# Optimization experiments

Hardware: AMD Instinct MI355X
Metric: run time of the kernel (lower is better)

The kernel has to match this reference:

```python
import jax, jax.numpy as jnp
import numpy as np
import math

D_MODEL = 1024
N_HEADS = 16
HEAD_DIM = D_MODEL // N_HEADS
B = 2
S = 2048

def setup_inputs() -> dict:
    key = jax.random.key(0)
    ks = jax.random.split(key, 5)
    x = jax.random.normal(ks[0], (B, S, D_MODEL), dtype=jnp.float32)
    # causal lower-triangular mask, broadcastable to [B, H, S, S]
    mask = jnp.tril(jnp.ones((S, S), dtype=bool))[None, None, :, :]
    # qkv_proj: Linear(d_model, 3*d_model); out_proj: Linear(d_model, d_model)
    lim_qkv = 1.0 / math.sqrt(D_MODEL)
    Wqkv = jax.random.uniform(ks[1], (D_MODEL, 3 * D_MODEL), minval=-lim_qkv, maxval=lim_qkv, dtype=jnp.float32)
    bqkv = jax.random.uniform(ks[2], (3 * D_MODEL,), minval=-lim_qkv, maxval=lim_qkv, dtype=jnp.float32)
    Wo = jax.random.uniform(ks[3], (D_MODEL, D_MODEL), minval=-lim_qkv, maxval=lim_qkv, dtype=jnp.float32)
    bo = jax.random.uniform(ks[4], (D_MODEL,), minval=-lim_qkv, maxval=lim_qkv, dtype=jnp.float32)
    return {"x": x, "mask": mask, "Wqkv": Wqkv, "bqkv": bqkv, "Wo": Wo, "bo": bo}

def reference(x, mask, Wqkv, bqkv, Wo, bo):
    b, s, d = x.shape
    scale = math.sqrt(HEAD_DIM)
    qkv = x @ Wqkv + bqkv                                   # [b, s, 3d]
    qkv = qkv.reshape(b, s, 3, N_HEADS, HEAD_DIM)
    qkv = jnp.transpose(qkv, (2, 0, 3, 1, 4))               # [3, b, h, s, hd]
    q, k, v = qkv[0], qkv[1], qkv[2]
    scores = jnp.einsum("bhqd,bhkd->bhqk", q, k) / scale    # [b, h, s, s]
    scores = jnp.where(mask, scores, -jnp.inf)
    attn = jax.nn.softmax(scores, axis=-1)                  # dropout inactive (eval)
    out = jnp.einsum("bhqk,bhkd->bhqd", attn, v)            # [b, h, s, hd]
    out = jnp.transpose(out, (0, 2, 1, 3)).reshape(b, s, d)
    return out @ Wo + bo
```

## Files before the change

### kernel.cpp

```cpp
#include <hip/hip_runtime.h>
#include <stdint.h>

typedef __bf16 bf16x8 __attribute__((ext_vector_type(8)));
typedef float  f32x4  __attribute__((ext_vector_type(4)));

__device__ __forceinline__ float bf2f(ushort u) {
    union { uint i; float f; } v; v.i = ((uint)u) << 16; return v.f;
}
__device__ __forceinline__ ushort f2bf(float f) {
    union { uint i; float f; } v; v.f = f;
    uint i = v.i;
    uint r = (i + 0x7fffu + ((i >> 16) & 1u)) >> 16;
    return (ushort)r;
}
__device__ __forceinline__ ushort f2bf_t(float f) {
    union { uint i; float f; } v; v.f = f;
    return (ushort)(v.i >> 16);
}

__device__ __forceinline__ void gld16(const ushort* g, ushort* l) {
    __builtin_amdgcn_global_load_lds((const __attribute__((address_space(1))) uint*)g,
                                     (__attribute__((address_space(3))) uint*)l, 16, 0, 0);
}

#define D_MODEL 1024
#define N_HEADS 16
#define HEAD_DIM 64
#define BATCH 2
#define SEQ 2048
#define M_ROWS (BATCH * SEQ)
#define N_ITEMS 1024
#define SCALE_LOG2E 0.18033688f

__global__ __launch_bounds__(256) void cast_f32_bf16(
    const float* __restrict__ in, ushort* __restrict__ out, int n4)
{
    int i = blockIdx.x * 256 + threadIdx.x;
    if (i < n4) {
        float4 v = ((const float4*)in)[i];
        ushort4 o;
        o.x = f2bf(v.x); o.y = f2bf(v.y); o.z = f2bf(v.z); o.w = f2bf(v.w);
        ((ushort4*)out)[i] = o;
    }
}

__global__ __launch_bounds__(256) void transpose_f32_bf16(
    const float* __restrict__ in, ushort* __restrict__ out, int K, int N)
{
    __shared__ float tile[64][65];
    const int k0 = blockIdx.y << 6, n0 = blockIdx.x << 6;
    const int tid = threadIdx.x;
    {
        const int r  = tid >> 4;
        const int c4 = (tid & 15) * 4;
#pragma unroll
        for (int rr = 0; rr < 4; ++rr) {
            int kk = r + rr * 16;
            float4 v = *(const float4*)(in + (size_t)(k0 + kk) * N + n0 + c4);
            tile[kk][c4 + 0] = v.x; tile[kk][c4 + 1] = v.y;
            tile[kk][c4 + 2] = v.z; tile[kk][c4 + 3] = v.w;
        }
    }
    __syncthreads();
    {
        const int nn = tid & 63;
        const int ch = tid >> 6;
#pragma unroll
        for (int cc = 0; cc < 2; ++cc) {
            int k8 = (ch + cc * 4) * 8;
            ushort tmp[8] __attribute__((aligned(16)));
#pragma unroll
            for (int j = 0; j < 8; ++j) tmp[j] = f2bf(tile[k8 + j][nn]);
            *(uint4*)(out + (size_t)(n0 + nn) * K + k0 + k8) = *(const uint4*)tmp;
        }
    }
}

__global__ __launch_bounds__(256) void gemm_bt128(
    const ushort* __restrict__ A, const ushort* __restrict__ Bt,
    const float* __restrict__ bias, float* __restrict__ out,
    ushort* __restrict__ Qb, ushort* __restrict__ Kb, ushort* __restrict__ Vb,
    int M, int N, int K, int mode)
{
    __shared__ ushort As[128 * 32];
    __shared__ ushort Bs[128 * 32];
    const int tid = threadIdx.x, lane = tid & 63, w = tid >> 6;
    const int wr = w >> 1, wc = w & 1;
    const int m0 = blockIdx.y * 128, n0 = blockIdx.x * 128;
    const int quad = lane >> 4, r15 = lane & 15, q8 = quad * 8;

    f32x4 acc[4][4] = {};

    const int cb0 = w * 64;
    const int cb1 = 256 + w * 64;
    const int c0 = cb0 + lane, c1 = cb1 + lane;
    const int row0 = c0 >> 2, sc0 = (c0 & 3) * 8;
    const int row1 = c1 >> 2, sc1 = (c1 & 3) * 8;

    for (int k0 = 0; k0 < K; k0 += 32) {
        gld16(A  + (size_t)(m0 + row0) * K + k0 + sc0, As + cb0 * 8);
        gld16(A  + (size_t)(m0 + row1) * K + k0 + sc1, As + cb1 * 8);
        gld16(Bt + (size_t)(n0 + row0) * K + k0 + sc0, Bs + cb0 * 8);
        gld16(Bt + (size_t)(n0 + row1) * K + k0 + sc1, Bs + cb1 * 8);
        __syncthreads();
        bf16x8 af[4], bfv[4];
#pragma unroll
        for (int mt = 0; mt < 4; ++mt)
            af[mt] = *(const bf16x8*)&As[(wr * 64 + mt * 16 + r15) * 32 + q8];
#pragma unroll
        for (int nt = 0; nt < 4; ++nt)
            bfv[nt] = *(const bf16x8*)&Bs[(wc * 64 + nt * 16 + r15) * 32 + q8];
#pragma unroll
        for (int mt = 0; mt < 4; ++mt)
#pragma unroll
            for (int nt = 0; nt < 4; ++nt)
                acc[mt][nt] = __builtin_amdgcn_mfma_f32_16x16x32_bf16(af[mt], bfv[nt], acc[mt][nt], 0, 0, 0);
        __syncthreads();
    }

    const int q4 = quad * 4;
    float bv[4];
#pragma unroll
    for (int nt = 0; nt < 4; ++nt) bv[nt] = bias[n0 + wc * 64 + nt * 16 + r15];
#pragma unroll
    for (int mt = 0; mt < 4; ++mt) {
#pragma unroll
        for (int nt = 0; nt < 4; ++nt) {
#pragma unroll
            for (int r = 0; r < 4; ++r) {
                int m = m0 + wr * 64 + mt * 16 + q4 + r;
                int n = n0 + wc * 64 + nt * 16 + r15;
                float v = acc[mt][nt][r] + bv[nt];
                if (mode == 0) {
                    int which = n >> 10, nh = n & 1023;
                    int h = nh >> 6, d = nh & 63;
                    int b = m >> 11, s = m & 2047;
                    size_t dst = (((size_t)(b * N_HEADS + h)) * SEQ + s) * HEAD_DIM + d;
                    ushort* p = (which == 0) ? Qb : ((which == 1) ? Kb : Vb);
                    p[dst] = f2bf(v);
                } else {
                    out[(size_t)m * N + n] = v;
                }
            }
        }
    }
}

__global__ __launch_bounds__(256) void attn_mfma(
    const ushort* __restrict__ Q, const ushort* __restrict__ K,
    const ushort* __restrict__ V, ushort* __restrict__ Out,
    int* __restrict__ counter)
{
    __shared__ ushort Ks[2][64 * 72];
    __shared__ ushort Vt[2][64 * 72];
    __shared__ ushort Ps[4][16 * 72];
    __shared__ int s_item;

    const int tid  = threadIdx.x;
    const int lane = tid & 63;
    const int w    = tid >> 6;
    const int quad = lane >> 4;
    const int r15  = lane & 15;
    const int q8   = quad * 8;

    const int srow = tid >> 2;
    const int scol = (tid & 3) * 16;
    const int kp = tid & 31;
    const int dg = tid >> 5;

    for (;;) {
        __syncthreads();
        if (tid == 0) s_item = atomicAdd(counter, 1);
        __syncthreads();
        const int item = s_item;
        if (item >= N_ITEMS) break;

        const int qblk = 31 - (item >> 5);
        const int bh   = item & 31;
        const int q0   = qblk * 64;
        const size_t base = (size_t)bh * SEQ * HEAD_DIM;
        const int wq0  = q0 + w * 16;
        const int ntiles = qblk + 1;

        bf16x8 qf[2];
        {
            const ushort* qrow = Q + base + (size_t)(wq0 + r15) * HEAD_DIM;
            qf[0] = *(const bf16x8*)(qrow + q8);
            qf[1] = *(const bf16x8*)(qrow + 32 + q8);
        }

        f32x4 o_acc[4] = {};
        float l_lane[4] = {0.f, 0.f, 0.f, 0.f};

        uint4 kr0, kr1, vr0, vr1;
        {
            const ushort* kpt = K + base + (size_t)srow * HEAD_DIM + scol;
            kr0 = *(const uint4*)kpt; kr1 = *(const uint4*)(kpt + 8);
            const ushort* vpt = V + base + (size_t)(2 * kp) * HEAD_DIM + dg * 8;
            vr0 = *(const uint4*)vpt; vr1 = *(const uint4*)(vpt + HEAD_DIM);
        }
        {
            ushort* ks = &Ks[0][0];
            *(uint4*)&ks[srow * 72 + scol]     = kr0;
            *(uint4*)&ks[srow * 72 + scol + 8] = kr1;
            const ushort* a = (const ushort*)&vr0;
            const ushort* b = (const ushort*)&vr1;
            uint* vt32 = (uint*)&Vt[0][0];
#pragma unroll
            for (int j = 0; j < 8; ++j)
                vt32[(dg * 8 + j) * 36 + ((kp + 4 * dg) & 31)] = (uint)a[j] | ((uint)b[j] << 16);
        }
        if (ntiles > 1) {
            const ushort* kpt = K + base + (size_t)(64 + srow) * HEAD_DIM + scol;
            kr0 = *(const uint4*)kpt; kr1 = *(const uint4*)(kpt + 8);
            const ushort* vpt = V + base + (size_t)(64 + 2 * kp) * HEAD_DIM + dg * 8;
            vr0 = *(const uint4*)vpt; vr1 = *(const uint4*)(vpt + HEAD_DIM);
        }

        for (int t = 0; t < ntiles; ++t) {
            __syncthreads();
            if (t + 1 < ntiles) {
                const int b1 = (t + 1) & 1;
                ushort* ks = &Ks[b1][0];
                *(uint4*)&ks[srow * 72 + scol]     = kr0;
                *(uint4*)&ks[srow * 72 + scol + 8] = kr1;
                const ushort* a = (const ushort*)&vr0;
                const ushort* b = (const ushort*)&vr1;
                uint* vt32 = (uint*)&Vt[b1][0];
#pragma unroll
                for (int j = 0; j < 8; ++j)
                    vt32[(dg * 8 + j) * 36 + ((kp + 4 * dg) & 31)] = (uint)a[j] | ((uint)b[j] << 16);
            }
            if (t + 2 < ntiles) {
                const int key2 = (t + 2) << 6;
                const ushort* kpt = K + base + (size_t)(key2 + srow) * HEAD_DIM + scol;
                kr0 = *(const uint4*)kpt; kr1 = *(const uint4*)(kpt + 8);
                const ushort* vpt = V + base + (size_t)(key2 + 2 * kp) * HEAD_DIM + dg * 8;
                vr0 = *(const uint4*)vpt; vr1 = *(const uint4*)(vpt + HEAD_DIM);
            }

            const ushort* KsB = &Ks[t & 1][0];
            const ushort* VtB = &Vt[t & 1][0];
            const bool diag = (t == ntiles - 1);
            const int ntmax = diag ? (w + 1) : 4;

            f32x4 s_acc[4];
#pragma unroll
            for (int nt = 0; nt < 4; ++nt) {
                if (nt >= ntmax) continue;
                f32x4 z = {};
#pragma unroll
                for (int ks = 0; ks < 2; ++ks) {
                    bf16x8 kf = *(const bf16x8*)&KsB[(nt * 16 + r15) * 72 + ks * 32 + q8];
                    z = __builtin_amdgcn_mfma_f32_16x16x32_bf16(qf[ks], kf, z, 0, 0, 0);
                }
                s_acc[nt] = z;
            }
#pragma unroll
            for (int nt = 0; nt < 4; ++nt) {
                if (nt >= ntmax) continue;
#pragma unroll
                for (int j = 0; j < 4; ++j) {
                    float e = exp2f(s_acc[nt][j] * SCALE_LOG2E);
                    if (diag && nt == w && r15 > quad * 4 + j) e = 0.f;
                    s_acc[nt][j] = e;
                    l_lane[j] += e;
                }
            }
            ushort* pb = &Ps[w][0];
#pragma unroll
            for (int nt = 0; nt < 4; ++nt)
#pragma unroll
                for (int j = 0; j < 4; ++j)
                    pb[(quad * 4 + j) * 72 + nt * 16 + r15] =
                        (nt < ntmax) ? f2bf_t(s_acc[nt][j]) : (ushort)0;
            bf16x8 pf0 = *(const bf16x8*)&pb[r15 * 72 + q8];
            bf16x8 pf1 = *(const bf16x8*)&pb[r15 * 72 + 32 + q8];

#pragma unroll
            for (int nt = 0; nt < 4; ++nt) {
                const int d0 = nt * 16 + r15;
                const int dsw = 4 * ((d0 >> 3) & 7);
                const int c0 = (4 * quad + dsw) & 31;
                const int c1 = (16 + 4 * quad + dsw) & 31;
                bf16x8 vf0 = *(const bf16x8*)&VtB[d0 * 72 + (c0 << 1)];
                bf16x8 vf1 = *(const bf16x8*)&VtB[d0 * 72 + (c1 << 1)];
                o_acc[nt] = __builtin_amdgcn_mfma_f32_16x16x32_bf16(pf0, vf0, o_acc[nt], 0, 0, 0);
                o_acc[nt] = __builtin_amdgcn_mfma_f32_16x16x32_bf16(pf1, vf1, o_acc[nt], 0, 0, 0);
            }
        }

        float l_f[4];
#pragma unroll
        for (int j = 0; j < 4; ++j) {
            float l = l_lane[j];
            l += __shfl_xor(l, 1);
            l += __shfl_xor(l, 2);
            l += __shfl_xor(l, 4);
            l += __shfl_xor(l, 8);
            l_f[j] = 1.f / l;
        }
        const int b = bh >> 4, h = bh & 15;
#pragma unroll
        for (int nt = 0; nt < 4; ++nt) {
#pragma unroll
            for (int j = 0; j < 4; ++j) {
                int qg = wq0 + quad * 4 + j;
                float v = o_acc[nt][j] * l_f[j];
                Out[((size_t)(b * SEQ + qg)) * D_MODEL + h * 64 + nt * 16 + r15] = f2bf(v);
            }
        }
    }
}

extern "C" void kernel_launch(void* const* d_in, const int* in_sizes, int n_in,
                              void* d_out, int out_size, void* d_ws, size_t ws_size,
                              hipStream_t stream)
{
    const float* x    = (const float*)d_in[0];
    const float* Wqkv = (const float*)d_in[2];
    const float* bqkv = (const float*)d_in[3];
    const float* Wo   = (const float*)d_in[4];
    const float* bo   = (const float*)d_in[5];
    float* out = (float*)d_out;

    char* ws = (char*)d_ws;
    size_t off = 0;
    ushort* xb    = (ushort*)(ws + off); off += (size_t)M_ROWS * D_MODEL * 2;
    ushort* WqkvT = (ushort*)(ws + off); off += (size_t)3 * D_MODEL * D_MODEL * 2;
    ushort* WoT   = (ushort*)(ws + off); off += (size_t)D_MODEL * D_MODEL * 2;
    const size_t qkv_elems = (size_t)BATCH * N_HEADS * SEQ * HEAD_DIM;
    ushort* Qb = (ushort*)(ws + off); off += qkv_elems * 2;
    ushort* Kb = (ushort*)(ws + off); off += qkv_elems * 2;
    ushort* Vb = (ushort*)(ws + off); off += qkv_elems * 2;
    ushort* attn_out = (ushort*)(ws + off); off += (size_t)M_ROWS * D_MODEL * 2;
    int* counter = (int*)(ws + off); off += 256;

    hipMemsetAsync(counter, 0, 4, stream);

    {
        int n4 = M_ROWS * D_MODEL / 4;
        cast_f32_bf16<<<(n4 + 255) / 256, 256, 0, stream>>>(x, xb, n4);
    }

    transpose_f32_bf16<<<dim3(3 * D_MODEL / 64, D_MODEL / 64), 256, 0, stream>>>(Wqkv, WqkvT, D_MODEL, 3 * D_MODEL);
    transpose_f32_bf16<<<dim3(D_MODEL / 64, D_MODEL / 64), 256, 0, stream>>>(Wo, WoT, D_MODEL, D_MODEL);

    gemm_bt128<<<dim3(3 * D_MODEL / 128, M_ROWS / 128), 256, 0, stream>>>(
        xb, WqkvT, bqkv, nullptr, Qb, Kb, Vb, M_ROWS, 3 * D_MODEL, D_MODEL, 0);

    attn_mfma<<<768, 256, 0, stream>>>(Qb, Kb, Vb, attn_out, counter);

    gemm_bt128<<<dim3(D_MODEL / 128, M_ROWS / 128), 256, 0, stream>>>(
        attn_out, WoT, bo, out, nullptr, nullptr, nullptr, M_ROWS, D_MODEL, D_MODEL, 1);
}
```

Baseline: 225.9 us.

## Use 128-row query blocks with 8 waves and split-KV for long rows

```diff
diff --git a/kernel.cpp b/kernel.cpp
--- a/kernel.cpp
+++ b/kernel.cpp
@@ -29,8 +29,8 @@
 #define BATCH 2
 #define SEQ 2048
 #define M_ROWS (BATCH * SEQ)
-#define N_ITEMS 1024
 #define SCALE_LOG2E 0.18033688f
+#define N_ITEMS 768
 
 __global__ __launch_bounds__(256) void cast_f32_bf16(
     const float* __restrict__ in, ushort* __restrict__ out, int n4)
@@ -146,14 +146,15 @@
     }
 }
 
-__global__ __launch_bounds__(256) void attn_mfma(
+__global__ __launch_bounds__(512, 4) void attn_mfma(
     const ushort* __restrict__ Q, const ushort* __restrict__ K,
     const ushort* __restrict__ V, ushort* __restrict__ Out,
+    float* __restrict__ Opart, float* __restrict__ lpart,
     int* __restrict__ counter)
 {
     __shared__ ushort Ks[2][64 * 72];
     __shared__ ushort Vt[2][64 * 72];
-    __shared__ ushort Ps[4][16 * 72];
+    __shared__ ushort Ps[8][16 * 72];
     __shared__ int s_item;
 
     const int tid  = threadIdx.x;
@@ -163,8 +164,8 @@
     const int r15  = lane & 15;
     const int q8   = quad * 8;
 
-    const int srow = tid >> 2;
-    const int scol = (tid & 3) * 16;
+    const int srow = tid >> 3;
+    const int scol = (tid & 7) * 8;
     const int kp = tid & 31;
     const int dg = tid >> 5;
 
@@ -175,12 +176,25 @@
         const int item = s_item;
         if (item >= N_ITEMS) break;
 
-        const int qblk = 31 - (item >> 5);
-        const int bh   = item & 31;
-        const int q0   = qblk * 64;
+        int p, bh, t0, t1, half;
+        if (item < 512) {
+            p = 15 - (item >> 6);
+            half = (item >> 5) & 1;
+            bh = item & 31;
+            const int hl = p + 1;
+            t0 = half * hl; t1 = t0 + hl;
+        } else {
+            const int j = item - 512;
+            p = 7 - (j >> 5);
+            bh = j & 31;
+            half = -1;
+            t0 = 0; t1 = 2 * p + 2;
+        }
+        const int ntf  = 2 * p + 2;
+        const int q0   = p * 128;
+        const int wq0  = q0 + w * 16;
+        const int tdiag = ntf - 2 + (w >> 2);
         const size_t base = (size_t)bh * SEQ * HEAD_DIM;
-        const int wq0  = q0 + w * 16;
-        const int ntiles = qblk + 1;
 
         bf16x8 qf[2];
         {
@@ -192,57 +206,59 @@
         f32x4 o_acc[4] = {};
         float l_lane[4] = {0.f, 0.f, 0.f, 0.f};
 
-        uint4 kr0, kr1, vr0, vr1;
+        uint4 kr; uint2 va, vb;
         {
-            const ushort* kpt = K + base + (size_t)srow * HEAD_DIM + scol;
-            kr0 = *(const uint4*)kpt; kr1 = *(const uint4*)(kpt + 8);
-            const ushort* vpt = V + base + (size_t)(2 * kp) * HEAD_DIM + dg * 8;
-            vr0 = *(const uint4*)vpt; vr1 = *(const uint4*)(vpt + HEAD_DIM);
+            const int key0 = t0 << 6;
+            const ushort* kpt = K + base + (size_t)(key0 + srow) * HEAD_DIM + scol;
+            kr = *(const uint4*)kpt;
+            const ushort* vpt = V + base + (size_t)(key0 + 2 * kp) * HEAD_DIM + dg * 4;
+            va = *(const uint2*)vpt; vb = *(const uint2*)(vpt + HEAD_DIM);
         }
         {
-            ushort* ks = &Ks[0][0];
-            *(uint4*)&ks[srow * 72 + scol]     = kr0;
-            *(uint4*)&ks[srow * 72 + scol + 8] = kr1;
-            const ushort* a = (const ushort*)&vr0;
-            const ushort* b = (const ushort*)&vr1;
-            uint* vt32 = (uint*)&Vt[0][0];
-#pragma unroll
-            for (int j = 0; j < 8; ++j)
-                vt32[(dg * 8 + j) * 36 + ((kp + 4 * dg) & 31)] = (uint)a[j] | ((uint)b[j] << 16);
-        }
-        if (ntiles > 1) {
-            const ushort* kpt = K + base + (size_t)(64 + srow) * HEAD_DIM + scol;
-            kr0 = *(const uint4*)kpt; kr1 = *(const uint4*)(kpt + 8);
-            const ushort* vpt = V + base + (size_t)(64 + 2 * kp) * HEAD_DIM + dg * 8;
-            vr0 = *(const uint4*)vpt; vr1 = *(const uint4*)(vpt + HEAD_DIM);
-        }
-
-        for (int t = 0; t < ntiles; ++t) {
+            ushort* ks = &Ks[t0 & 1][0];
+            *(uint4*)&ks[srow * 72 + scol] = kr;
+            const ushort* ap = (const ushort*)&va;
+            const ushort* bp = (const ushort*)&vb;
+            uint* vt32 = (uint*)&Vt[t0 & 1][0];
+#pragma unroll
+            for (int j = 0; j < 4; ++j)
+                vt32[(dg * 4 + j) * 36 + kp] = (uint)ap[j] | ((uint)bp[j] << 16);
+        }
+        if (t0 + 1 < t1) {
+            const int key0 = (t0 + 1) << 6;
+            const ushort* kpt = K + base + (size_t)(key0 + srow) * HEAD_DIM + scol;
+            kr = *(const uint4*)kpt;
+            const ushort* vpt = V + base + (size_t)(key0 + 2 * kp) * HEAD_DIM + dg * 4;
+            va = *(const uint2*)vpt; vb = *(const uint2*)(vpt + HEAD_DIM);
+        }
+
+        for (int t = t0; t < t1; ++t) {
             __syncthreads();
-            if (t + 1 < ntiles) {
+            if (t + 1 < t1) {
                 const int b1 = (t + 1) & 1;
                 ushort* ks = &Ks[b1][0];
-                *(uint4*)&ks[srow * 72 + scol]     = kr0;
-                *(uint4*)&ks[srow * 72 + scol + 8] = kr1;
-                const ushort* a = (const ushort*)&vr0;
-                const ushort* b = (const ushort*)&vr1;
+                *(uint4*)&ks[srow * 72 + scol] = kr;
+                const ushort* ap = (const ushort*)&va;
+                const ushort* bp = (const ushort*)&vb;
                 uint* vt32 = (uint*)&Vt[b1][0];
 #pragma unroll
-                for (int j = 0; j < 8; ++j)
-                    vt32[(dg * 8 + j) * 36 + ((kp + 4 * dg) & 31)] = (uint)a[j] | ((uint)b[j] << 16);
-            }
-            if (t + 2 < ntiles) {
+                for (int j = 0; j < 4; ++j)
+                    vt32[(dg * 4 + j) * 36 + kp] = (uint)ap[j] | ((uint)bp[j] << 16);
+            }
+            if (t + 2 < t1) {
                 const int key2 = (t + 2) << 6;
                 const ushort* kpt = K + base + (size_t)(key2 + srow) * HEAD_DIM + scol;
-                kr0 = *(const uint4*)kpt; kr1 = *(const uint4*)(kpt + 8);
-                const ushort* vpt = V + base + (size_t)(key2 + 2 * kp) * HEAD_DIM + dg * 8;
-                vr0 = *(const uint4*)vpt; vr1 = *(const uint4*)(vpt + HEAD_DIM);
-            }
+                kr = *(const uint4*)kpt;
+                const ushort* vpt = V + base + (size_t)(key2 + 2 * kp) * HEAD_DIM + dg * 4;
+                va = *(const uint2*)vpt; vb = *(const uint2*)(vpt + HEAD_DIM);
+            }
+
+            const int ntmax = (t < tdiag) ? 4 : ((t == tdiag) ? (w & 3) + 1 : 0);
+            if (ntmax == 0) continue;
 
             const ushort* KsB = &Ks[t & 1][0];
             const ushort* VtB = &Vt[t & 1][0];
-            const bool diag = (t == ntiles - 1);
-            const int ntmax = diag ? (w + 1) : 4;
+            const bool diag = (t == tdiag);
 
             f32x4 s_acc[4];
 #pragma unroll
@@ -262,7 +278,7 @@
 #pragma unroll
                 for (int j = 0; j < 4; ++j) {
                     float e = exp2f(s_acc[nt][j] * SCALE_LOG2E);
-                    if (diag && nt == w && r15 > quad * 4 + j) e = 0.f;
+                    if (diag && nt == (w & 3) && r15 > quad * 4 + j) e = 0.f;
                     s_acc[nt][j] = e;
                     l_lane[j] += e;
                 }
@@ -280,17 +296,14 @@
 #pragma unroll
             for (int nt = 0; nt < 4; ++nt) {
                 const int d0 = nt * 16 + r15;
-                const int dsw = 4 * ((d0 >> 3) & 7);
-                const int c0 = (4 * quad + dsw) & 31;
-                const int c1 = (16 + 4 * quad + dsw) & 31;
-                bf16x8 vf0 = *(const bf16x8*)&VtB[d0 * 72 + (c0 << 1)];
-                bf16x8 vf1 = *(const bf16x8*)&VtB[d0 * 72 + (c1 << 1)];
+                bf16x8 vf0 = *(const bf16x8*)&VtB[d0 * 72 + q8];
+                bf16x8 vf1 = *(const bf16x8*)&VtB[d0 * 72 + 32 + q8];
                 o_acc[nt] = __builtin_amdgcn_mfma_f32_16x16x32_bf16(pf0, vf0, o_acc[nt], 0, 0, 0);
                 o_acc[nt] = __builtin_amdgcn_mfma_f32_16x16x32_bf16(pf1, vf1, o_acc[nt], 0, 0, 0);
             }
         }
 
-        float l_f[4];
+        float lsum[4];
 #pragma unroll
         for (int j = 0; j < 4; ++j) {
             float l = l_lane[j];
@@ -298,19 +311,58 @@
             l += __shfl_xor(l, 2);
             l += __shfl_xor(l, 4);
             l += __shfl_xor(l, 8);
-            l_f[j] = 1.f / l;
-        }
-        const int b = bh >> 4, h = bh & 15;
-#pragma unroll
-        for (int nt = 0; nt < 4; ++nt) {
-#pragma unroll
-            for (int j = 0; j < 4; ++j) {
-                int qg = wq0 + quad * 4 + j;
-                float v = o_acc[nt][j] * l_f[j];
-                Out[((size_t)(b * SEQ + qg)) * D_MODEL + h * 64 + nt * 16 + r15] = f2bf(v);
-            }
-        }
-    }
+            lsum[j] = l;
+        }
+        if (half < 0) {
+            const int b = bh >> 4, h = bh & 15;
+#pragma unroll
+            for (int nt = 0; nt < 4; ++nt) {
+#pragma unroll
+                for (int j = 0; j < 4; ++j) {
+                    int qg = wq0 + quad * 4 + j;
+                    float v = o_acc[nt][j] / lsum[j];
+                    Out[((size_t)(b * SEQ + qg)) * D_MODEL + h * 64 + nt * 16 + r15] = f2bf(v);
+                }
+            }
+        } else {
+            const int qrb = wq0 - 1024;
+            float* Ob = Opart + ((size_t)(half * 32 + bh) * 1024) * 64;
+#pragma unroll
+            for (int nt = 0; nt < 4; ++nt)
+#pragma unroll
+                for (int j = 0; j < 4; ++j)
+                    Ob[(size_t)(qrb + quad * 4 + j) * 64 + nt * 16 + r15] = o_acc[nt][j];
+            if (r15 == 0) {
+                float* lb = lpart + (size_t)(half * 32 + bh) * 1024;
+#pragma unroll
+                for (int j = 0; j < 4; ++j)
+                    lb[qrb + quad * 4 + j] = lsum[j];
+            }
+        }
+    }
+}
+
+__global__ __launch_bounds__(256) void attn_combine(
+    const float* __restrict__ Opart, const float* __restrict__ lpart,
+    ushort* __restrict__ Out)
+{
+    const int idx = blockIdx.x * 256 + threadIdx.x;
+    const int bh = idx >> 14;
+    const int rem = idx & 16383;
+    const int qrel = rem >> 4, d4 = (rem & 15) * 4;
+    const size_t o0 = ((size_t)bh * 1024 + qrel) * 64 + d4;
+    const size_t o1 = ((size_t)(32 + bh) * 1024 + qrel) * 64 + d4;
+    float4 a = *(const float4*)(Opart + o0);
+    float4 c = *(const float4*)(Opart + o1);
+    float l = lpart[bh * 1024 + qrel] + lpart[32 * 1024 + bh * 1024 + qrel];
+    float inv = 1.f / l;
+    ushort4 r;
+    r.x = f2bf((a.x + c.x) * inv);
+    r.y = f2bf((a.y + c.y) * inv);
+    r.z = f2bf((a.z + c.z) * inv);
+    r.w = f2bf((a.w + c.w) * inv);
+    const int b = bh >> 4, h = bh & 15;
+    *(ushort4*)(Out + ((size_t)(b * SEQ + 1024 + qrel)) * D_MODEL + h * 64 + d4) = r;
 }
 
 extern "C" void kernel_launch(void* const* d_in, const int* in_sizes, int n_in,
@@ -334,6 +386,8 @@
     ushort* Kb = (ushort*)(ws + off); off += qkv_elems * 2;
     ushort* Vb = (ushort*)(ws + off); off += qkv_elems * 2;
     ushort* attn_out = (ushort*)(ws + off); off += (size_t)M_ROWS * D_MODEL * 2;
+    float* Opart = (float*)(ws + off); off += (size_t)2 * 32 * 1024 * 64 * 4;
+    float* lpart = (float*)(ws + off); off += (size_t)2 * 32 * 1024 * 4;
     int* counter = (int*)(ws + off); off += 256;
 
     hipMemsetAsync(counter, 0, 4, stream);
@@ -349,7 +403,9 @@
     gemm_bt128<<<dim3(3 * D_MODEL / 128, M_ROWS / 128), 256, 0, stream>>>(
         xb, WqkvT, bqkv, nullptr, Qb, Kb, Vb, M_ROWS, 3 * D_MODEL, D_MODEL, 0);
 
-    attn_mfma<<<768, 256, 0, stream>>>(Qb, Kb, Vb, attn_out, counter);
+    attn_mfma<<<512, 512, 0, stream>>>(Qb, Kb, Vb, attn_out, Opart, lpart, counter);
+
+    attn_combine<<<2048, 256, 0, stream>>>(Opart, lpart, attn_out);
 
     gemm_bt128<<<dim3(D_MODEL / 128, M_ROWS / 128), 256, 0, stream>>>(
         attn_out, WoT, bo, out, nullptr, nullptr, nullptr, M_ROWS, D_MODEL, D_MODEL, 1);
```

Result: slower. 247.1 us (+9.4%).
